# Kernel optimization log

Measured on AMD Instinct MI355X. Metric: run time of the kernel, lower is better.

The kernel has to match this reference:

```python
import jax, jax.numpy as jnp
import numpy as np

B, T, E, D = 32, 8192, 256, 32  # batch, seq, embed_dim, output_dim
H, M = D, 2 * D                 # SSM hidden_dim, mlp_dim


def _ssm_block(x, Win, bin_, log_a, Wout, bout, W1, b1, W2, b2):
    """Diagonal linear SSM scan + residual MLP. x: (B,T,D) -> (B,T,D)."""
    u = x @ Win + bin_                      # (B,T,H)
    a = jax.nn.sigmoid(log_a)               # (H,) per-channel decay in (0,1)
    aa = jnp.broadcast_to(a, u.shape)

    def comb(c1, c2):
        a1, h1 = c1
        a2, h2 = c2
        return a1 * a2, a2 * h1 + h2

    _, h = jax.lax.associative_scan(comb, (aa, u), axis=1)  # h_t = a*h_{t-1} + u_t
    y = h @ Wout + bout                      # (B,T,D)
    return y + jax.nn.gelu(y @ W1 + b1) @ W2 + b2


def setup_inputs() -> dict:
    key = jax.random.key(0)
    ks = jax.random.split(key, 20)
    s_in, s_d, s_m = 1.0 / np.sqrt(E), 1.0 / np.sqrt(D), 1.0 / np.sqrt(M)
    inp = {
        "e_seq": jax.random.normal(ks[0], (B, T, E), dtype=jnp.float32),
        "Wpi": jax.random.normal(ks[1], (E, D), dtype=jnp.float32) * s_in,
        "bpi": jnp.zeros((D,), jnp.float32),
        "Wpo": jax.random.normal(ks[2], (2 * D, D), dtype=jnp.float32) * s_d,
        "bpo": jnp.zeros((D,), jnp.float32),
    }
    for i, pfx in enumerate(["f", "b"]):
        o = 3 + 8 * i
        inp[pfx + "_Win"] = jax.random.normal(ks[o], (D, H), dtype=jnp.float32) * s_d
        inp[pfx + "_bin"] = jnp.zeros((H,), jnp.float32)
        inp[pfx + "_loga"] = jax.random.normal(ks[o + 1], (H,), dtype=jnp.float32)
        inp[pfx + "_Wout"] = jax.random.normal(ks[o + 2], (H, D), dtype=jnp.float32) * s_d
        inp[pfx + "_bout"] = jnp.zeros((D,), jnp.float32)
        inp[pfx + "_W1"] = jax.random.normal(ks[o + 3], (D, M), dtype=jnp.float32) * s_d
        inp[pfx + "_b1"] = jnp.zeros((M,), jnp.float32)
        inp[pfx + "_W2"] = jax.random.normal(ks[o + 4], (M, D), dtype=jnp.float32) * s_m
        inp[pfx + "_b2"] = jnp.zeros((D,), jnp.float32)
    return inp


def reference(e_seq, Wpi, bpi, Wpo, bpo,
              f_Win, f_bin, f_loga, f_Wout, f_bout, f_W1, f_b1, f_W2, f_b2,
              b_Win, b_bin, b_loga, b_Wout, b_bout, b_W1, b_b1, b_W2, b_b2):
    x = e_seq @ Wpi + bpi                                    # (B,T,D)
    fwd = _ssm_block(x, f_Win, f_bin, f_loga, f_Wout, f_bout, f_W1, f_b1, f_W2, f_b2)
    bwd = _ssm_block(x[:, ::-1], b_Win, b_bin, b_loga, b_Wout, b_bout,
                     b_W1, b_b1, b_W2, b_b2)[:, ::-1]
    combined = jnp.concatenate([fwd, bwd], axis=-1)           # (B,T,2D)
    return combined @ Wpo + bpo                               # (B,T,D)
```

## Files before the change

kernel.cpp:

```cpp
#include <hip/hip_runtime.h>


typedef unsigned short u16;
typedef unsigned int   u32;
typedef __bf16 bf16x8 __attribute__((ext_vector_type(8)));
typedef float  f32x4  __attribute__((ext_vector_type(4)));

constexpr int BB = 32, TT = 8192, NCH = 64;
constexpr int BT = BB * TT;
constexpr int LCH = 256;
constexpr int NCHUNK = TT / LCH;

#define MFMA16(av, bv, cc) __builtin_amdgcn_mfma_f32_16x16x32_bf16((av), (bv), (cc), 0, 0, 0)

__device__ __forceinline__ u16 f2bf(float x) {
    union { float f; u32 u; } v; v.f = x;
    u32 r = (v.u + 0x7FFFu + ((v.u >> 16) & 1u)) >> 16;
    return (u16)r;
}
__device__ __forceinline__ float bf2f(u16 x) {
    union { u32 u; float f; } v; v.u = ((u32)x) << 16;
    return v.f;
}
__device__ __forceinline__ float gelu_tanh(float x) {
    float inner = 0.7978845608028654f * fmaf(0.044715f * x, x * x, x);
    float ez = __expf(2.f * inner);
    float t = 1.f - 2.f / (ez + 1.f);
    return 0.5f * x * (1.f + t);
}

__global__ void k0_prep(const float* __restrict__ Wpi, const float* __restrict__ bpi,
                        const float* __restrict__ fWin, const float* __restrict__ fbin,
                        const float* __restrict__ floga,
                        const float* __restrict__ bWin, const float* __restrict__ bbin,
                        const float* __restrict__ bloga,
                        const float* __restrict__ fW1, const float* __restrict__ bW1,
                        const float* __restrict__ fW2, const float* __restrict__ bW2,
                        const float* __restrict__ fb2, const float* __restrict__ bb2,
                        const float* __restrict__ fWout, const float* __restrict__ bWout,
                        const float* __restrict__ Wpo, const float* __restrict__ bpo,
                        u16* __restrict__ WuT, float* __restrict__ bu,
                        float* __restrict__ a_arr, float* __restrict__ l2a,
                        u16* __restrict__ W1Tbf, u16* __restrict__ W2poCatT,
                        u16* __restrict__ WoutTbf, u16* __restrict__ WpoCatT,
                        float* __restrict__ bc)
{
    const int blk = blockIdx.x, tid = threadIdx.x;
    if (blk < 64) {
        const float* Win = (blk < 32) ? fWin : bWin;
        const int nn = blk & 31;
        float s = 0.f;
        #pragma unroll
        for (int d = 0; d < 32; ++d) s = fmaf(Wpi[tid * 32 + d], Win[d * 32 + nn], s);
        WuT[blk * 256 + tid] = f2bf(s);
        if (tid == 0) {
            const float* bin = (blk < 32) ? fbin : bbin;
            float sb = bin[nn];
            for (int d = 0; d < 32; ++d) sb = fmaf(bpi[d], Win[d * 32 + nn], sb);
            bu[blk] = sb;
        }
    } else if (blk == 64) {
        if (tid < 64) {
            const float* lg = (tid < 32) ? floga : bloga;
            float a = 1.f / (1.f + __expf(-lg[tid & 31]));
            a_arr[tid] = a;
            l2a[tid] = log2f(a);
        } else if (tid < 96) {
            int i = tid - 64;
            float s = bpo[i];
            for (int d = 0; d < 32; ++d) s = fmaf(fb2[d], Wpo[d * 32 + i], s);
            for (int d = 0; d < 32; ++d) s = fmaf(bb2[d], Wpo[(32 + d) * 32 + i], s);
            bc[i] = s;
        }
    } else if (blk == 65 || blk == 66) {
        int dir = blk - 65;
        const float* W1 = dir ? bW1 : fW1;
        for (int x = tid; x < 2048; x += 256) {
            int n = x >> 5, k = x & 31;
            W1Tbf[dir * 2048 + n * 32 + k] = f2bf(W1[k * 64 + n]);
        }
    } else if (blk == 67 || blk == 68) {
        int dir = blk - 67;
        const float* W2 = dir ? bW2 : fW2;
        const float* Wp = Wpo + dir * 32 * 32;
        for (int x = tid; x < 2048; x += 256) {
            int j = x >> 5, i = x & 31;
            float s = 0.f;
            for (int d = 0; d < 32; ++d) s = fmaf(W2[j * 32 + d], Wp[d * 32 + i], s);
            W2poCatT[i * 128 + dir * 64 + j] = f2bf(s);
        }
    } else if (blk == 69 || blk == 70) {
        int dir = blk - 69;
        const float* Wout = dir ? bWout : fWout;
        for (int x = tid; x < 1024; x += 256) {
            int n = x >> 5, k = x & 31;
            WoutTbf[dir * 1024 + n * 32 + k] = f2bf(Wout[k * 32 + n]);
        }
    } else {
        for (int x = tid; x < 2048; x += 256) {
            int n = x >> 6, k = x & 63;
            WpoCatT[n * 64 + k] = f2bf(Wpo[k * 32 + n]);
        }
    }
}

__global__ __launch_bounds__(256) void kA_proj_scan(const float* __restrict__ e,
    const u16* __restrict__ WuT, const float* __restrict__ bu,
    const float* __restrict__ a_arr, const float* __restrict__ l2a,
    u16* __restrict__ h, float* __restrict__ Ebuf)
{
    __shared__ __align__(16) u16 As[32][264];
    __shared__ __align__(16) u16 utile[256 * 64];
    __shared__ float eSub[64][4];
    const int tid = threadIdx.x;
    const int blk = blockIdx.x;
    const size_t t0 = (size_t)blk * 256;
    const int lane = tid & 63, wave = tid >> 6;
    const int row16 = lane & 15, quad = lane >> 4;
    const int wr = (wave & 1) * 16;
    const int wc = (wave >> 1) * 32;

    #pragma unroll 1
    for (int s = 0; s < 8; ++s) {
        const float4* eg = reinterpret_cast<const float4*>(e + (t0 + s * 32) * 256);
        #pragma unroll
        for (int it = 0; it < 8; ++it) {
            int i = tid + it * 256;
            int r = i >> 6, kk = (i & 63) << 2;
            float4 v = eg[i];
            uint2 pk;
            pk.x = (u32)f2bf(v.x) | ((u32)f2bf(v.y) << 16);
            pk.y = (u32)f2bf(v.z) | ((u32)f2bf(v.w) << 16);
            *reinterpret_cast<uint2*>(&As[r][kk]) = pk;
        }
        __syncthreads();
        f32x4 acc[2] = {{0.f,0.f,0.f,0.f},{0.f,0.f,0.f,0.f}};
        #pragma unroll
        for (int ks = 0; ks < 8; ++ks) {
            bf16x8 av = *reinterpret_cast<const bf16x8*>(&As[wr + row16][ks * 32 + quad * 8]);
            #pragma unroll
            for (int c2 = 0; c2 < 2; ++c2) {
                bf16x8 bv = *reinterpret_cast<const bf16x8*>(WuT + (wc + c2 * 16 + row16) * 256 + ks * 32 + quad * 8);
                acc[c2] = MFMA16(av, bv, acc[c2]);
            }
        }
        #pragma unroll
        for (int c2 = 0; c2 < 2; ++c2) {
            int col = wc + c2 * 16 + row16;
            float bias = bu[col];
            #pragma unroll
            for (int r = 0; r < 4; ++r) {
                int trow = s * 32 + wr + quad * 4 + r;
                utile[trow * 64 + col] = f2bf(acc[c2][r] + bias);
            }
        }
        __syncthreads();
    }

    const int ch = tid & 63, sid = tid >> 6;
    const float a = a_arr[ch];
    const bool fwd = (ch < 32);
    float hh = 0.f;
    if (fwd) {
        for (int i = 0; i < 64; ++i) { int t = sid * 64 + i;
            hh = fmaf(a, hh, bf2f(utile[t * 64 + ch])); utile[t * 64 + ch] = f2bf(hh); }
    } else {
        for (int i = 63; i >= 0; --i) { int t = sid * 64 + i;
            hh = fmaf(a, hh, bf2f(utile[t * 64 + ch])); utile[t * 64 + ch] = f2bf(hh); }
    }
    eSub[ch][sid] = hh;
    __syncthreads();
    const float A = exp2f(64.f * l2a[ch]);
    float cin = 0.f;
    if (fwd) { for (int j = 0; j < sid; ++j) cin = fmaf(A, cin, eSub[ch][j]); }
    else     { for (int j = 3; j > sid; --j) cin = fmaf(A, cin, eSub[ch][j]); }
    if (fwd && sid == 3)  Ebuf[(size_t)blk * 64 + ch] = fmaf(A, cin, eSub[ch][3]);
    if (!fwd && sid == 0) Ebuf[(size_t)blk * 64 + ch] = fmaf(A, cin, eSub[ch][0]);
    float p = cin;
    if (fwd) {
        for (int i = 0; i < 64; ++i) { int t = sid * 64 + i; p *= a;
            utile[t * 64 + ch] = f2bf(bf2f(utile[t * 64 + ch]) + p); }
    } else {
        for (int i = 63; i >= 0; --i) { int t = sid * 64 + i; p *= a;
            utile[t * 64 + ch] = f2bf(bf2f(utile[t * 64 + ch]) + p); }
    }
    __syncthreads();
    uint4* gw = reinterpret_cast<uint4*>(h + t0 * 64);
    const uint4* s4 = reinterpret_cast<const uint4*>(utile);
    #pragma unroll
    for (int i = 0; i < 8; ++i) gw[tid + 256 * i] = s4[tid + 256 * i];
}

__global__ void k3_carry(const float* __restrict__ Ebuf, float* __restrict__ Cin,
                         const float* __restrict__ l2a)
{
    int tid = blockIdx.x * 256 + threadIdx.x;
    if (tid >= BB * NCH) return;
    int b = tid >> 6, ch = tid & 63;
    float aL = exp2f((float)LCH * l2a[ch]);
    float S = 0.f;
    if (ch < 32) {
        for (int c = 0; c < NCHUNK; ++c) {
            size_t idx = ((size_t)(b * NCHUNK + c)) * 64 + ch;
            Cin[idx] = S; S = fmaf(aL, S, Ebuf[idx]);
        }
    } else {
        for (int c = NCHUNK - 1; c >= 0; --c) {
            size_t idx = ((size_t)(b * NCHUNK + c)) * 64 + ch;
            Cin[idx] = S; S = fmaf(aL, S, Ebuf[idx]);
        }
    }
}

__global__ __launch_bounds__(256) void kB_out(const u16* __restrict__ h,
    const float* __restrict__ Cin, const float* __restrict__ l2a,
    const u16* __restrict__ WoutTbf, const float* __restrict__ fbout, const float* __restrict__ bbout,
    const u16* __restrict__ W1Tbf, const float* __restrict__ fb1, const float* __restrict__ bb1,
    const u16* __restrict__ WpoCatT, const u16* __restrict__ W2poCatT,
    const float* __restrict__ bc, float* __restrict__ out)
{
    __shared__ __align__(16) u16 Yt[256 * 64];
    __shared__ __align__(16) u16 Zw[4][16 * 128];
    const int tid = threadIdx.x;
    const int blk = blockIdx.x;
    const size_t t0 = (size_t)blk * 256;
    const int lane = tid & 63, wave = tid >> 6;
    const int row16 = lane & 15, quad = lane >> 4;
    const float* cinp = Cin + (size_t)blk * 64;

    #pragma unroll 1
    for (int rr = 0; rr < 4; ++rr) {
        const int rt = wave * 4 + rr;
        const int kpos = rt * 16 + row16;
        #pragma unroll
        for (int dir = 0; dir < 2; ++dir) {
            uint4 hv = *reinterpret_cast<const uint4*>(h + (t0 + kpos) * 64 + dir * 32 + quad * 8);
            u32 hw[4] = {hv.x, hv.y, hv.z, hv.w};
            const float off = dir ? (float)(LCH - kpos) : (float)(kpos + 1);
            union { bf16x8 v; u16 s[8]; } af;
            #pragma unroll
            for (int j = 0; j < 8; ++j) {
                int chn = dir * 32 + quad * 8 + j;
                float f = bf2f((u16)((hw[j >> 1] >> ((j & 1) * 16)) & 0xFFFFu));
                f = fmaf(cinp[chn], exp2f(off * l2a[chn]), f);
                af.s[j] = f2bf(f);
            }
            f32x4 yv[2] = {{0.f,0.f,0.f,0.f},{0.f,0.f,0.f,0.f}};
            #pragma unroll
            for (int nt = 0; nt < 2; ++nt) {
                bf16x8 bv = *reinterpret_cast<const bf16x8*>(WoutTbf + dir * 1024 + (nt * 16 + row16) * 32 + quad * 8);
                yv[nt] = MFMA16(af.v, bv, yv[nt]);
            }
            const float* boutp = dir ? bbout : fbout;
            #pragma unroll
            for (int nt = 0; nt < 2; ++nt) {
                float bb = boutp[nt * 16 + row16];
                #pragma unroll
                for (int r = 0; r < 4; ++r) {
                    int row = rt * 16 + quad * 4 + r;
                    int col = dir * 32 + nt * 16 + row16;
                    int cs = (col >> 3) ^ (row & 7);
                    Yt[row * 64 + cs * 8 + (col & 7)] = f2bf(yv[nt][r] + bb);
                }
            }
        }
    }

    #pragma unroll 1
    for (int rr = 0; rr < 4; ++rr) {
        const int rt = wave * 4 + rr;
        const int arow = rt * 16 + row16;
        f32x4 o0 = {0.f,0.f,0.f,0.f}, o1 = {0.f,0.f,0.f,0.f};

        #pragma unroll
        for (int kb = 0; kb < 2; ++kb) {
            int cs = (kb * 4 + quad) ^ (arow & 7);
            bf16x8 av = *reinterpret_cast<const bf16x8*>(&Yt[arow * 64 + cs * 8]);
            bf16x8 bv0 = *reinterpret_cast<const bf16x8*>(WpoCatT + (row16) * 64 + kb * 32 + quad * 8);
            bf16x8 bv1 = *reinterpret_cast<const bf16x8*>(WpoCatT + (16 + row16) * 64 + kb * 32 + quad * 8);
            o0 = MFMA16(av, bv0, o0);
            o1 = MFMA16(av, bv1, o1);
        }
        #pragma unroll
        for (int dir = 0; dir < 2; ++dir) {
            int cs = (dir * 4 + quad) ^ (arow & 7);
            bf16x8 av = *reinterpret_cast<const bf16x8*>(&Yt[arow * 64 + cs * 8]);
            const float* b1p = dir ? bb1 : fb1;
            #pragma unroll
            for (int nt2 = 0; nt2 < 4; ++nt2) {
                f32x4 z = {0.f,0.f,0.f,0.f};
                bf16x8 bv = *reinterpret_cast<const bf16x8*>(W1Tbf + dir * 2048 + (nt2 * 16 + row16) * 32 + quad * 8);
                z = MFMA16(av, bv, z);
                float bb = b1p[nt2 * 16 + row16];
                #pragma unroll
                for (int r = 0; r < 4; ++r) {
                    float zz = gelu_tanh(z[r] + bb);
                    int zrow = quad * 4 + r;
                    int zcol = dir * 64 + nt2 * 16 + row16;
                    int zcs = (zcol >> 3) ^ (zrow & 7);
                    Zw[wave][zrow * 128 + zcs * 8 + (zcol & 7)] = f2bf(zz);
                }
            }
        }
        #pragma unroll
        for (int kb = 0; kb < 4; ++kb) {
            int zcs = (kb * 4 + quad) ^ (row16 & 7);
            bf16x8 av = *reinterpret_cast<const bf16x8*>(&Zw[wave][row16 * 128 + zcs * 8]);
            bf16x8 bv0 = *reinterpret_cast<const bf16x8*>(W2poCatT + (row16) * 128 + kb * 32 + quad * 8);
            bf16x8 bv1 = *reinterpret_cast<const bf16x8*>(W2poCatT + (16 + row16) * 128 + kb * 32 + quad * 8);
            o0 = MFMA16(av, bv0, o0);
            o1 = MFMA16(av, bv1, o1);
        }
        #pragma unroll
        for (int r = 0; r < 4; ++r) {
            size_t row = t0 + rt * 16 + quad * 4 + r;
            out[row * 32 + row16]      = o0[r] + bc[row16];
            out[row * 32 + 16 + row16] = o1[r] + bc[16 + row16];
        }
    }
}

extern "C" void kernel_launch(void* const* d_in, const int* in_sizes, int n_in,
                              void* d_out, int out_size, void* d_ws, size_t ws_size,
                              hipStream_t stream)
{
    (void)in_sizes; (void)n_in; (void)out_size; (void)ws_size;
    const float* e     = (const float*)d_in[0];
    const float* Wpi   = (const float*)d_in[1];
    const float* bpi   = (const float*)d_in[2];
    const float* Wpo   = (const float*)d_in[3];
    const float* bpo   = (const float*)d_in[4];
    const float* fWin  = (const float*)d_in[5];
    const float* fbin  = (const float*)d_in[6];
    const float* floga = (const float*)d_in[7];
    const float* fWout = (const float*)d_in[8];
    const float* fbout = (const float*)d_in[9];
    const float* fW1   = (const float*)d_in[10];
    const float* fb1   = (const float*)d_in[11];
    const float* fW2   = (const float*)d_in[12];
    const float* fb2   = (const float*)d_in[13];
    const float* bWin  = (const float*)d_in[14];
    const float* bbin  = (const float*)d_in[15];
    const float* bloga = (const float*)d_in[16];
    const float* bWout = (const float*)d_in[17];
    const float* bbout = (const float*)d_in[18];
    const float* bW1   = (const float*)d_in[19];
    const float* bb1   = (const float*)d_in[20];
    const float* bW2   = (const float*)d_in[21];
    const float* bb2   = (const float*)d_in[22];
    float* outp = (float*)d_out;

    char* ws = (char*)d_ws;
    size_t off = 0;
    auto walloc = [&](size_t bytes) { void* p = ws + off; off += (bytes + 255) & ~(size_t)255; return p; };
    u16*   hbuf  = (u16*)  walloc((size_t)BT * 64 * 2);
    u16*   WuT   = (u16*)  walloc(64 * 256 * 2);
    float* bu    = (float*)walloc(64 * 4);
    float* a_arr = (float*)walloc(64 * 4);
    float* l2a   = (float*)walloc(64 * 4);
    float* Ebuf  = (float*)walloc((size_t)BB * NCHUNK * 64 * 4);
    float* Cin   = (float*)walloc((size_t)BB * NCHUNK * 64 * 4);
    u16*   W1Tbf    = (u16*)walloc(2 * 64 * 32 * 2);
    u16*   W2poCatT = (u16*)walloc(32 * 128 * 2);
    u16*   WoutTbf  = (u16*)walloc(2 * 32 * 32 * 2);
    u16*   WpoCatT  = (u16*)walloc(32 * 64 * 2);
    float* bc    = (float*)walloc(32 * 4);

    k0_prep<<<72, 256, 0, stream>>>(Wpi, bpi, fWin, fbin, floga, bWin, bbin, bloga,
                                    fW1, bW1, fW2, bW2, fb2, bb2, fWout, bWout, Wpo, bpo,
                                    WuT, bu, a_arr, l2a, W1Tbf, W2poCatT, WoutTbf, WpoCatT, bc);
    kA_proj_scan<<<BB * NCHUNK, 256, 0, stream>>>(e, WuT, bu, a_arr, l2a, hbuf, Ebuf);
    k3_carry<<<8, 256, 0, stream>>>(Ebuf, Cin, l2a);
    kB_out<<<BB * NCHUNK, 256, 0, stream>>>(hbuf, Cin, l2a,
                                            WoutTbf, fbout, bbout,
                                            W1Tbf, fb1, bb1,
                                            WpoCatT, W2poCatT, bc, outp);
}
```

Measured before the change: 463.4 us.

## Load projection operands directly per wave, widen in-block scan, hoist carry powers

The projection stage drops the shared-memory staging tile and its per-step barriers. Each wave now loads its own 64 rows of e straight from global memory into MFMA operands and computes all 64 output columns. The in-block scan handles two channels per thread with packed 32-bit LDS access over eight 32-step segments instead of four 64-step ones, which shortens the serial chain. In the output kernel, the per-element exp2 for the carry term is replaced by a running product with a precomputed a^16 per channel, which adds a new prep output and rounding from repeated multiplication.

```diff
diff --git a/kernel.cpp b/kernel.cpp
--- a/kernel.cpp
+++ b/kernel.cpp
@@ -41,6 +41,7 @@
                         const float* __restrict__ Wpo, const float* __restrict__ bpo,
                         u16* __restrict__ WuT, float* __restrict__ bu,
                         float* __restrict__ a_arr, float* __restrict__ l2a,
+                        float* __restrict__ a16p,
                         u16* __restrict__ W1Tbf, u16* __restrict__ W2poCatT,
                         u16* __restrict__ WoutTbf, u16* __restrict__ WpoCatT,
                         float* __restrict__ bc)
@@ -63,8 +64,10 @@
         if (tid < 64) {
             const float* lg = (tid < 32) ? floga : bloga;
             float a = 1.f / (1.f + __expf(-lg[tid & 31]));
+            float l2 = log2f(a);
             a_arr[tid] = a;
-            l2a[tid] = log2f(a);
+            l2a[tid] = l2;
+            a16p[tid] = exp2f(16.f * l2);
         } else if (tid < 96) {
             int i = tid - 64;
             float s = bpo[i];
@@ -109,80 +112,116 @@
     const float* __restrict__ a_arr, const float* __restrict__ l2a,
     u16* __restrict__ h, float* __restrict__ Ebuf)
 {
-    __shared__ __align__(16) u16 As[32][264];
     __shared__ __align__(16) u16 utile[256 * 64];
-    __shared__ float eSub[64][4];
+    __shared__ float eSub[8][64];
     const int tid = threadIdx.x;
     const int blk = blockIdx.x;
     const size_t t0 = (size_t)blk * 256;
     const int lane = tid & 63, wave = tid >> 6;
     const int row16 = lane & 15, quad = lane >> 4;
-    const int wr = (wave & 1) * 16;
-    const int wc = (wave >> 1) * 32;
 
     #pragma unroll 1
-    for (int s = 0; s < 8; ++s) {
-        const float4* eg = reinterpret_cast<const float4*>(e + (t0 + s * 32) * 256);
-        #pragma unroll
-        for (int it = 0; it < 8; ++it) {
-            int i = tid + it * 256;
-            int r = i >> 6, kk = (i & 63) << 2;
-            float4 v = eg[i];
-            uint2 pk;
-            pk.x = (u32)f2bf(v.x) | ((u32)f2bf(v.y) << 16);
-            pk.y = (u32)f2bf(v.z) | ((u32)f2bf(v.w) << 16);
-            *reinterpret_cast<uint2*>(&As[r][kk]) = pk;
-        }
-        __syncthreads();
-        f32x4 acc[2] = {{0.f,0.f,0.f,0.f},{0.f,0.f,0.f,0.f}};
+    for (int rt = 0; rt < 4; ++rt) {
+        const int trow0 = wave * 64 + rt * 16;
+        const float* erow = e + (t0 + trow0 + row16) * 256;
+        f32x4 acc[4] = {{0.f,0.f,0.f,0.f},{0.f,0.f,0.f,0.f},{0.f,0.f,0.f,0.f},{0.f,0.f,0.f,0.f}};
         #pragma unroll
         for (int ks = 0; ks < 8; ++ks) {
-            bf16x8 av = *reinterpret_cast<const bf16x8*>(&As[wr + row16][ks * 32 + quad * 8]);
-            #pragma unroll
-            for (int c2 = 0; c2 < 2; ++c2) {
-                bf16x8 bv = *reinterpret_cast<const bf16x8*>(WuT + (wc + c2 * 16 + row16) * 256 + ks * 32 + quad * 8);
-                acc[c2] = MFMA16(av, bv, acc[c2]);
-            }
-        }
-        #pragma unroll
-        for (int c2 = 0; c2 < 2; ++c2) {
-            int col = wc + c2 * 16 + row16;
+            float4 a0 = *reinterpret_cast<const float4*>(erow + ks * 32 + quad * 8);
+            float4 a1 = *reinterpret_cast<const float4*>(erow + ks * 32 + quad * 8 + 4);
+            union { bf16x8 v; u16 s[8]; } af;
+            af.s[0] = f2bf(a0.x); af.s[1] = f2bf(a0.y);
+            af.s[2] = f2bf(a0.z); af.s[3] = f2bf(a0.w);
+            af.s[4] = f2bf(a1.x); af.s[5] = f2bf(a1.y);
+            af.s[6] = f2bf(a1.z); af.s[7] = f2bf(a1.w);
+            #pragma unroll
+            for (int ct = 0; ct < 4; ++ct) {
+                bf16x8 bv = *reinterpret_cast<const bf16x8*>(WuT + (ct * 16 + row16) * 256 + ks * 32 + quad * 8);
+                acc[ct] = MFMA16(af.v, bv, acc[ct]);
+            }
+        }
+        #pragma unroll
+        for (int ct = 0; ct < 4; ++ct) {
+            int col = ct * 16 + row16;
             float bias = bu[col];
             #pragma unroll
             for (int r = 0; r < 4; ++r) {
-                int trow = s * 32 + wr + quad * 4 + r;
-                utile[trow * 64 + col] = f2bf(acc[c2][r] + bias);
-            }
-        }
-        __syncthreads();
-    }
-
-    const int ch = tid & 63, sid = tid >> 6;
-    const float a = a_arr[ch];
-    const bool fwd = (ch < 32);
-    float hh = 0.f;
+                int trow = trow0 + quad * 4 + r;
+                utile[trow * 64 + col] = f2bf(acc[ct][r] + bias);
+            }
+        }
+    }
+
+    const int c2 = tid & 31, sid = tid >> 5;
+    const int ch0 = c2 * 2, ch1 = ch0 + 1;
+    const bool fwd = (ch0 < 32);
+    const float a0 = a_arr[ch0], a1 = a_arr[ch1];
+    u32* ut32 = reinterpret_cast<u32*>(utile);
+
+    float h0 = 0.f, h1 = 0.f;
     if (fwd) {
-        for (int i = 0; i < 64; ++i) { int t = sid * 64 + i;
-            hh = fmaf(a, hh, bf2f(utile[t * 64 + ch])); utile[t * 64 + ch] = f2bf(hh); }
+        for (int i = 0; i < 32; ++i) {
+            int t = sid * 32 + i;
+            u32 w = ut32[t * 32 + c2];
+            h0 = fmaf(a0, h0, bf2f((u16)(w & 0xFFFFu)));
+            h1 = fmaf(a1, h1, bf2f((u16)(w >> 16)));
+            ut32[t * 32 + c2] = (u32)f2bf(h0) | ((u32)f2bf(h1) << 16);
+        }
     } else {
-        for (int i = 63; i >= 0; --i) { int t = sid * 64 + i;
-            hh = fmaf(a, hh, bf2f(utile[t * 64 + ch])); utile[t * 64 + ch] = f2bf(hh); }
-    }
-    eSub[ch][sid] = hh;
+        for (int i = 31; i >= 0; --i) {
+            int t = sid * 32 + i;
+            u32 w = ut32[t * 32 + c2];
+            h0 = fmaf(a0, h0, bf2f((u16)(w & 0xFFFFu)));
+            h1 = fmaf(a1, h1, bf2f((u16)(w >> 16)));
+            ut32[t * 32 + c2] = (u32)f2bf(h0) | ((u32)f2bf(h1) << 16);
+        }
+    }
+    eSub[sid][ch0] = h0;
+    eSub[sid][ch1] = h1;
     __syncthreads();
-    const float A = exp2f(64.f * l2a[ch]);
-    float cin = 0.f;
-    if (fwd) { for (int j = 0; j < sid; ++j) cin = fmaf(A, cin, eSub[ch][j]); }
-    else     { for (int j = 3; j > sid; --j) cin = fmaf(A, cin, eSub[ch][j]); }
-    if (fwd && sid == 3)  Ebuf[(size_t)blk * 64 + ch] = fmaf(A, cin, eSub[ch][3]);
-    if (!fwd && sid == 0) Ebuf[(size_t)blk * 64 + ch] = fmaf(A, cin, eSub[ch][0]);
-    float p = cin;
+
+    const float A0 = exp2f(32.f * l2a[ch0]);
+    const float A1 = exp2f(32.f * l2a[ch1]);
+    float cin0 = 0.f, cin1 = 0.f;
     if (fwd) {
-        for (int i = 0; i < 64; ++i) { int t = sid * 64 + i; p *= a;
-            utile[t * 64 + ch] = f2bf(bf2f(utile[t * 64 + ch]) + p); }
+        for (int j = 0; j < sid; ++j) {
+            cin0 = fmaf(A0, cin0, eSub[j][ch0]);
+            cin1 = fmaf(A1, cin1, eSub[j][ch1]);
+        }
     } else {
-        for (int i = 63; i >= 0; --i) { int t = sid * 64 + i; p *= a;
-            utile[t * 64 + ch] = f2bf(bf2f(utile[t * 64 + ch]) + p); }
+        for (int j = 7; j > sid; --j) {
+            cin0 = fmaf(A0, cin0, eSub[j][ch0]);
+            cin1 = fmaf(A1, cin1, eSub[j][ch1]);
+        }
+    }
+    if (fwd && sid == 7) {
+        Ebuf[(size_t)blk * 64 + ch0] = fmaf(A0, cin0, eSub[7][ch0]);
+        Ebuf[(size_t)blk * 64 + ch1] = fmaf(A1, cin1, eSub[7][ch1]);
+    }
+    if (!fwd && sid == 0) {
+        Ebuf[(size_t)blk * 64 + ch0] = fmaf(A0, cin0, eSub[0][ch0]);
+        Ebuf[(size_t)blk * 64 + ch1] = fmaf(A1, cin1, eSub[0][ch1]);
+    }
+
+    float p0 = cin0, p1 = cin1;
+    if (fwd) {
+        for (int i = 0; i < 32; ++i) {
+            int t = sid * 32 + i;
+            p0 *= a0; p1 *= a1;
+            u32 w = ut32[t * 32 + c2];
+            float v0 = bf2f((u16)(w & 0xFFFFu)) + p0;
+            float v1 = bf2f((u16)(w >> 16)) + p1;
+            ut32[t * 32 + c2] = (u32)f2bf(v0) | ((u32)f2bf(v1) << 16);
+        }
+    } else {
+        for (int i = 31; i >= 0; --i) {
+            int t = sid * 32 + i;
+            p0 *= a0; p1 *= a1;
+            u32 w = ut32[t * 32 + c2];
+            float v0 = bf2f((u16)(w & 0xFFFFu)) + p0;
+            float v1 = bf2f((u16)(w >> 16)) + p1;
+            ut32[t * 32 + c2] = (u32)f2bf(v0) | ((u32)f2bf(v1) << 16);
+        }
     }
     __syncthreads();
     uint4* gw = reinterpret_cast<uint4*>(h + t0 * 64);
@@ -214,6 +253,7 @@
 
 __global__ __launch_bounds__(256) void kB_out(const u16* __restrict__ h,
     const float* __restrict__ Cin, const float* __restrict__ l2a,
+    const float* __restrict__ a16p,
     const u16* __restrict__ WoutTbf, const float* __restrict__ fbout, const float* __restrict__ bbout,
     const u16* __restrict__ W1Tbf, const float* __restrict__ fb1, const float* __restrict__ bb1,
     const u16* __restrict__ WpoCatT, const u16* __restrict__ W2poCatT,
@@ -228,22 +268,31 @@
     const int row16 = lane & 15, quad = lane >> 4;
     const float* cinp = Cin + (size_t)blk * 64;
 
-    #pragma unroll 1
-    for (int rr = 0; rr < 4; ++rr) {
-        const int rt = wave * 4 + rr;
-        const int kpos = rt * 16 + row16;
-        #pragma unroll
-        for (int dir = 0; dir < 2; ++dir) {
+    #pragma unroll
+    for (int dir = 0; dir < 2; ++dir) {
+        const float* boutp = dir ? bbout : fbout;
+        float pw[8], A16[8];
+        #pragma unroll
+        for (int j = 0; j < 8; ++j) {
+            const int chn = dir * 32 + quad * 8 + j;
+            A16[j] = a16p[chn];
+            const float off0 = dir ? (float)(256 - wave * 64 - 48 - row16)
+                                   : (float)(wave * 64 + row16 + 1);
+            pw[j] = exp2f(off0 * l2a[chn]) * cinp[chn];
+        }
+        #pragma unroll 1
+        for (int rri = 0; rri < 4; ++rri) {
+            const int rr = dir ? (3 - rri) : rri;
+            const int rt = wave * 4 + rr;
+            const int kpos = rt * 16 + row16;
             uint4 hv = *reinterpret_cast<const uint4*>(h + (t0 + kpos) * 64 + dir * 32 + quad * 8);
             u32 hw[4] = {hv.x, hv.y, hv.z, hv.w};
-            const float off = dir ? (float)(LCH - kpos) : (float)(kpos + 1);
             union { bf16x8 v; u16 s[8]; } af;
             #pragma unroll
             for (int j = 0; j < 8; ++j) {
-                int chn = dir * 32 + quad * 8 + j;
-                float f = bf2f((u16)((hw[j >> 1] >> ((j & 1) * 16)) & 0xFFFFu));
-                f = fmaf(cinp[chn], exp2f(off * l2a[chn]), f);
+                float f = bf2f((u16)((hw[j >> 1] >> ((j & 1) * 16)) & 0xFFFFu)) + pw[j];
                 af.s[j] = f2bf(f);
+                pw[j] *= A16[j];
             }
             f32x4 yv[2] = {{0.f,0.f,0.f,0.f},{0.f,0.f,0.f,0.f}};
             #pragma unroll
@@ -251,7 +300,6 @@
                 bf16x8 bv = *reinterpret_cast<const bf16x8*>(WoutTbf + dir * 1024 + (nt * 16 + row16) * 32 + quad * 8);
                 yv[nt] = MFMA16(af.v, bv, yv[nt]);
             }
-            const float* boutp = dir ? bbout : fbout;
             #pragma unroll
             for (int nt = 0; nt < 2; ++nt) {
                 float bb = boutp[nt * 16 + row16];
@@ -358,6 +406,7 @@
     float* bu    = (float*)walloc(64 * 4);
     float* a_arr = (float*)walloc(64 * 4);
     float* l2a   = (float*)walloc(64 * 4);
+    float* a16p  = (float*)walloc(64 * 4);
     float* Ebuf  = (float*)walloc((size_t)BB * NCHUNK * 64 * 4);
     float* Cin   = (float*)walloc((size_t)BB * NCHUNK * 64 * 4);
     u16*   W1Tbf    = (u16*)walloc(2 * 64 * 32 * 2);
@@ -368,10 +417,10 @@
 
     k0_prep<<<72, 256, 0, stream>>>(Wpi, bpi, fWin, fbin, floga, bWin, bbin, bloga,
                                     fW1, bW1, fW2, bW2, fb2, bb2, fWout, bWout, Wpo, bpo,
-                                    WuT, bu, a_arr, l2a, W1Tbf, W2poCatT, WoutTbf, WpoCatT, bc);
+                                    WuT, bu, a_arr, l2a, a16p, W1Tbf, W2poCatT, WoutTbf, WpoCatT, bc);
     kA_proj_scan<<<BB * NCHUNK, 256, 0, stream>>>(e, WuT, bu, a_arr, l2a, hbuf, Ebuf);
     k3_carry<<<8, 256, 0, stream>>>(Ebuf, Cin, l2a);
-    kB_out<<<BB * NCHUNK, 256, 0, stream>>>(hbuf, Cin, l2a,
+    kB_out<<<BB * NCHUNK, 256, 0, stream>>>(hbuf, Cin, l2a, a16p,
                                             WoutTbf, fbout, bbout,
                                             W1Tbf, fb1, bb1,
                                             WpoCatT, W2poCatT, bc, outp);
```

Result: slower. 479.5 us (+3.5%).
